# Kernel tuning notes

Measured on AMD Instinct MI355X. Metric: run time of the kernel, lower is better.

## Reference

```python
import jax, jax.numpy as jnp
import numpy as np

N_NODES = 16384   # n_nodes
N_LINKS = 8192    # batch of target links
D_EMB = 128       # embedding dim
EDGE_P = 0.004    # adjacency density -> avg degree ~65


def setup_inputs() -> dict:
    key = jax.random.key(0)
    k1, k2, k3 = jax.random.split(key, 3)
    adj = jax.random.bernoulli(k1, EDGE_P, (N_NODES, N_NODES))
    adj = adj | adj.T                      # symmetric graph
    adj = adj & ~jnp.eye(N_NODES, dtype=bool)  # no self loops
    links = jax.random.randint(k2, (N_LINKS, 2), 0, N_NODES)
    emb = jax.random.normal(k3, (N_NODES, D_EMB), dtype=jnp.float32)
    return {"targetLink": links, "adjacent": adj, "NodeEmbedding": emb}


def reference(targetLink, adjacent, NodeEmbedding):
    # targetLink: [B,2] int, adjacent: [N,N] bool, NodeEmbedding: [N,D] float
    i = targetLink[:, 0]
    j = targetLink[:, 1]
    emb_i = NodeEmbedding[i]               # [B,D] gather
    emb_j = NodeEmbedding[j]               # [B,D] gather
    product = emb_i * emb_j                # [B,D]
    # common-neighbor indicator: u is a CN of (i,j) iff adj[i,u] and adj[j,u]
    cn_mask = (adjacent[i] & adjacent[j]).astype(NodeEmbedding.dtype)  # [B,N]
    # sum of embeddings over common neighbors (fused gather-reduce)
    cn_sum = cn_mask @ NodeEmbedding       # [B,D]
    return jnp.concatenate([product, cn_sum], axis=-1)  # [B,2D]
```

## Files before the change

### kernel.cpp

```cpp
#include <hip/hip_runtime.h>

#define N_NODES 16384
#define D_EMB   128
#define LIST_CAP 1024
#define BM_U64   256
#define FLAG_OFF N_NODES
#define BM_OFF_BYTES (1 << 17)
#define WS_NEEDED (BM_OFF_BYTES + (size_t)N_NODES * (BM_U64 * 8))

__global__ __launch_bounds__(256) void init_kernel(
    const unsigned int* __restrict__ words, int* __restrict__ flags)
{
    if (blockIdx.x < 64) {
        flags[blockIdx.x * 256 + threadIdx.x] = 0;
    } else {
        __shared__ int s_any;
        if (threadIdx.x == 0) s_any = 0;
        __syncthreads();
        int any = 0;
        for (int k = threadIdx.x; k < 16384; k += 256)
            if (words[k] > 1u) any = 1;
        if (any) atomicOr(&s_any, 1);
        __syncthreads();
        if (threadIdx.x == 0) flags[FLAG_OFF] = s_any;
    }
}

__global__ __launch_bounds__(256) void claim_compress_kernel(
    const int* __restrict__ links, const void* __restrict__ adjv,
    int* __restrict__ flags, unsigned long long* __restrict__ bm64,
    int n_endpoints)
{
    const int e = blockIdx.x;
    if (e >= n_endpoints) return;
    const int r = links[e];

    __shared__ int s_claimed;
    if (threadIdx.x == 0)
        s_claimed = (atomicCAS(&flags[r], 0, 1) == 0) ? 1 : 0;
    __syncthreads();
    if (!s_claimed) return;

    const int t = threadIdx.x;
    const int byte_layout = flags[FLAG_OFF];

    if (!byte_layout) {
        const uint4* row = reinterpret_cast<const uint4*>(
            (const int*)adjv + (size_t)r * N_NODES);
        unsigned int lo = 0u, hi = 0u;
#pragma unroll
        for (int k = 0; k < 8; ++k) {
            const uint4 v = row[k * 256 + t];
            const unsigned int nib = min(v.x, 1u) | (min(v.y, 1u) << 1)
                                   | (min(v.z, 1u) << 2) | (min(v.w, 1u) << 3);
            lo |= nib << (4 * k);
        }
#pragma unroll
        for (int k = 8; k < 16; ++k) {
            const uint4 v = row[k * 256 + t];
            const unsigned int nib = min(v.x, 1u) | (min(v.y, 1u) << 1)
                                   | (min(v.z, 1u) << 2) | (min(v.w, 1u) << 3);
            hi |= nib << (4 * (k - 8));
        }
        bm64[(size_t)r * BM_U64 + t] = ((unsigned long long)hi << 32) | lo;
    } else {
        const uint4* row = reinterpret_cast<const uint4*>(
            (const unsigned char*)adjv + (size_t)r * N_NODES);
        unsigned long long bits = 0ull;
#pragma unroll
        for (int q = 0; q < 4; ++q) {
            const uint4 v = row[t * 4 + q];
            const unsigned int arr[4] = {v.x, v.y, v.z, v.w};
#pragma unroll
            for (int a = 0; a < 4; ++a)
#pragma unroll
                for (int bb = 0; bb < 4; ++bb)
                    if ((arr[a] >> (8 * bb)) & 0xFFu)
                        bits |= 1ull << (q * 16 + a * 4 + bb);
        }
        bm64[(size_t)r * BM_U64 + t] = bits;
    }
}

__global__ __launch_bounds__(256) void link_kernel(
    const int* __restrict__ links, const unsigned long long* __restrict__ bm64,
    const float* __restrict__ emb, float* __restrict__ out,
    const int* __restrict__ flags, int n_links)
{
    const int link = blockIdx.x;
    if (link >= n_links) return;
    const int i = links[2 * link];
    const int j = links[2 * link + 1];
    const int byte_layout = flags[FLAG_OFF];

    __shared__ int s_list[LIST_CAP];
    __shared__ int s_count;
    if (threadIdx.x == 0) s_count = 0;
    __syncthreads();

    const int t = threadIdx.x;
    unsigned long long m = bm64[(size_t)i * BM_U64 + t]
                         & bm64[(size_t)j * BM_U64 + t];
    while (m) {
        const int b = __ffsll(m) - 1;
        m &= m - 1;
        const int node = byte_layout
            ? (t * 64 + b)
            : (((b >> 2) << 10) + (t << 2) + (b & 3));
        const int pos = atomicAdd(&s_count, 1);
        if (pos < LIST_CAP) s_list[pos] = node;
    }
    __syncthreads();

    int count = s_count;
    if (count > LIST_CAP) count = LIST_CAP;

    const size_t obase = (size_t)link * (2 * D_EMB);
    if (t < D_EMB) {
        out[obase + t] = emb[(size_t)i * D_EMB + t] * emb[(size_t)j * D_EMB + t];
    } else {
        const int d = t - D_EMB;
        float s = 0.0f;
        for (int c = 0; c < count; ++c)
            s += emb[(size_t)s_list[c] * D_EMB + d];
        out[obase + D_EMB + d] = s;
    }
}

__global__ __launch_bounds__(256) void detect_layout_kernel(
    const unsigned int* __restrict__ words, int* __restrict__ flag)
{
    __shared__ int s_any;
    if (threadIdx.x == 0) s_any = 0;
    __syncthreads();
    int any = 0;
    for (int k = threadIdx.x; k < 16384; k += 256)
        if (words[k] > 1u) any = 1;
    if (any) atomicOr(&s_any, 1);
    __syncthreads();
    if (threadIdx.x == 0) *flag = s_any;
}

__global__ __launch_bounds__(256) void ncn_direct(
    const int* __restrict__ links, const void* __restrict__ adjv,
    const float* __restrict__ emb, float* __restrict__ out,
    const int* __restrict__ flag, int n_links)
{
    const int link = blockIdx.x;
    if (link >= n_links) return;
    const int i = links[2 * link];
    const int j = links[2 * link + 1];

    __shared__ int s_list[LIST_CAP];
    __shared__ int s_count;
    if (threadIdx.x == 0) s_count = 0;
    __syncthreads();

    const int byte_layout = flag ? flag[0] : 0;
    if (byte_layout) {
        const uint4* rowi = reinterpret_cast<const uint4*>(
            (const unsigned char*)adjv + (size_t)i * N_NODES);
        const uint4* rowj = reinterpret_cast<const uint4*>(
            (const unsigned char*)adjv + (size_t)j * N_NODES);
#pragma unroll
        for (int c = 0; c < 4; ++c) {
            const int idx = c * 256 + threadIdx.x;
            const uint4 a = rowi[idx];
            const uint4 bq = rowj[idx];
            unsigned int m[4] = {a.x & bq.x, a.y & bq.y, a.z & bq.z, a.w & bq.w};
            if (m[0] | m[1] | m[2] | m[3]) {
                const int base = idx * 16;
#pragma unroll
                for (int w = 0; w < 4; ++w) {
                    unsigned int v = m[w];
                    if (!v) continue;
#pragma unroll
                    for (int b8 = 0; b8 < 4; ++b8) {
                        if ((v >> (8 * b8)) & 0xFFu) {
                            int pos = atomicAdd(&s_count, 1);
                            if (pos < LIST_CAP) s_list[pos] = base + w * 4 + b8;
                        }
                    }
                }
            }
        }
    } else {
        const uint4* rowi = reinterpret_cast<const uint4*>(
            (const int*)adjv + (size_t)i * N_NODES);
        const uint4* rowj = reinterpret_cast<const uint4*>(
            (const int*)adjv + (size_t)j * N_NODES);
#pragma unroll
        for (int c = 0; c < 16; ++c) {
            const int idx = c * 256 + threadIdx.x;
            const uint4 a = rowi[idx];
            const uint4 bq = rowj[idx];
            const int base = idx * 4;
            if (a.x & bq.x) { int p = atomicAdd(&s_count, 1); if (p < LIST_CAP) s_list[p] = base + 0; }
            if (a.y & bq.y) { int p = atomicAdd(&s_count, 1); if (p < LIST_CAP) s_list[p] = base + 1; }
            if (a.z & bq.z) { int p = atomicAdd(&s_count, 1); if (p < LIST_CAP) s_list[p] = base + 2; }
            if (a.w & bq.w) { int p = atomicAdd(&s_count, 1); if (p < LIST_CAP) s_list[p] = base + 3; }
        }
    }
    __syncthreads();

    int count = s_count;
    if (count > LIST_CAP) count = LIST_CAP;

    const int t = threadIdx.x;
    const size_t obase = (size_t)link * (2 * D_EMB);
    if (t < D_EMB) {
        out[obase + t] = emb[(size_t)i * D_EMB + t] * emb[(size_t)j * D_EMB + t];
    } else {
        const int d = t - D_EMB;
        float s = 0.0f;
        for (int c = 0; c < count; ++c)
            s += emb[(size_t)s_list[c] * D_EMB + d];
        out[obase + D_EMB + d] = s;
    }
}

extern "C" void kernel_launch(void* const* d_in, const int* in_sizes, int n_in,
                              void* d_out, int out_size, void* d_ws, size_t ws_size,
                              hipStream_t stream) {
    const int* links = (const int*)d_in[0];
    const void* adj = d_in[1];
    const float* emb = (const float*)d_in[2];
    float* out = (float*)d_out;

    const int n_links = in_sizes[0] / 2;

    if (ws_size >= WS_NEEDED) {
        int* flags = (int*)d_ws;
        unsigned long long* bm64 =
            (unsigned long long*)((char*)d_ws + BM_OFF_BYTES);

        init_kernel<<<65, 256, 0, stream>>>((const unsigned int*)adj, flags);
        claim_compress_kernel<<<2 * n_links, 256, 0, stream>>>(
            links, adj, flags, bm64, 2 * n_links);
        link_kernel<<<n_links, 256, 0, stream>>>(
            links, bm64, emb, out, flags, n_links);
    } else {
        int* flag = (ws_size >= sizeof(int)) ? (int*)d_ws : nullptr;
        if (flag) detect_layout_kernel<<<1, 256, 0, stream>>>(
            (const unsigned int*)adj, flag);
        ncn_direct<<<n_links, 256, 0, stream>>>(links, adj, emb, out, flag, n_links);
    }
}
```

Before: 178.1 us.

## Compact unique endpoint rows into a list and compress two rows per block

Replaces the per-endpoint claim-and-compress blocks with a thread-level marking kernel that appends unique row IDs to a workspace list. A second kernel then compresses two adjacency rows per block into bitmaps. This removes the many blocks that previously launched only to exit, and doubles the outstanding loads per thread. It adds an extra launch, and blocks beyond the unique count still launch and exit.

```diff
diff --git a/kernel.cpp b/kernel.cpp
--- a/kernel.cpp
+++ b/kernel.cpp
@@ -5,17 +5,19 @@
 #define LIST_CAP 1024
 #define BM_U64   256
 #define FLAG_OFF N_NODES
-#define BM_OFF_BYTES (1 << 17)
+#define CNT_OFF  (N_NODES + 1)
+#define LIST_OFF (N_NODES + 8)
+#define BM_OFF_BYTES (1 << 18)
 #define WS_NEEDED (BM_OFF_BYTES + (size_t)N_NODES * (BM_U64 * 8))
 
-__global__ __launch_bounds__(256) void init_kernel(
+__global__ __launch_bounds__(256) void zero_probe_kernel(
     const unsigned int* __restrict__ words, int* __restrict__ flags)
 {
     if (blockIdx.x < 64) {
         flags[blockIdx.x * 256 + threadIdx.x] = 0;
     } else {
         __shared__ int s_any;
-        if (threadIdx.x == 0) s_any = 0;
+        if (threadIdx.x == 0) { s_any = 0; flags[CNT_OFF] = 0; }
         __syncthreads();
         int any = 0;
         for (int k = threadIdx.x; k < 16384; k += 256)
@@ -26,59 +28,88 @@
     }
 }
 
-__global__ __launch_bounds__(256) void claim_compress_kernel(
-    const int* __restrict__ links, const void* __restrict__ adjv,
-    int* __restrict__ flags, unsigned long long* __restrict__ bm64,
-    int n_endpoints)
-{
-    const int e = blockIdx.x;
+__global__ __launch_bounds__(256) void mark_list_kernel(
+    const int* __restrict__ links, int* __restrict__ flags, int n_endpoints)
+{
+    const int e = blockIdx.x * 256 + threadIdx.x;
     if (e >= n_endpoints) return;
     const int r = links[e];
-
-    __shared__ int s_claimed;
-    if (threadIdx.x == 0)
-        s_claimed = (atomicCAS(&flags[r], 0, 1) == 0) ? 1 : 0;
-    __syncthreads();
-    if (!s_claimed) return;
-
+    if (atomicCAS(&flags[r], 0, 1) == 0) {
+        const int pos = atomicAdd(&flags[CNT_OFF], 1);
+        flags[LIST_OFF + pos] = r;
+    }
+}
+
+__global__ __launch_bounds__(256) void compress_pair_kernel(
+    const void* __restrict__ adjv, const int* __restrict__ flags,
+    unsigned long long* __restrict__ bm64)
+{
+    const int n_used = flags[CNT_OFF];
+    const int i0 = 2 * blockIdx.x;
+    const int i1 = i0 + 1;
+    if (i0 >= n_used) return;
+    const int r0 = flags[LIST_OFF + i0];
+    const int r1 = (i1 < n_used) ? flags[LIST_OFF + i1] : -1;
     const int t = threadIdx.x;
     const int byte_layout = flags[FLAG_OFF];
 
     if (!byte_layout) {
-        const uint4* row = reinterpret_cast<const uint4*>(
-            (const int*)adjv + (size_t)r * N_NODES);
-        unsigned int lo = 0u, hi = 0u;
-#pragma unroll
-        for (int k = 0; k < 8; ++k) {
-            const uint4 v = row[k * 256 + t];
-            const unsigned int nib = min(v.x, 1u) | (min(v.y, 1u) << 1)
-                                   | (min(v.z, 1u) << 2) | (min(v.w, 1u) << 3);
-            lo |= nib << (4 * k);
-        }
-#pragma unroll
-        for (int k = 8; k < 16; ++k) {
-            const uint4 v = row[k * 256 + t];
-            const unsigned int nib = min(v.x, 1u) | (min(v.y, 1u) << 1)
-                                   | (min(v.z, 1u) << 2) | (min(v.w, 1u) << 3);
-            hi |= nib << (4 * (k - 8));
-        }
-        bm64[(size_t)r * BM_U64 + t] = ((unsigned long long)hi << 32) | lo;
-    } else {
-        const uint4* row = reinterpret_cast<const uint4*>(
-            (const unsigned char*)adjv + (size_t)r * N_NODES);
-        unsigned long long bits = 0ull;
-#pragma unroll
-        for (int q = 0; q < 4; ++q) {
-            const uint4 v = row[t * 4 + q];
-            const unsigned int arr[4] = {v.x, v.y, v.z, v.w};
-#pragma unroll
-            for (int a = 0; a < 4; ++a)
-#pragma unroll
-                for (int bb = 0; bb < 4; ++bb)
-                    if ((arr[a] >> (8 * bb)) & 0xFFu)
-                        bits |= 1ull << (q * 16 + a * 4 + bb);
-        }
-        bm64[(size_t)r * BM_U64 + t] = bits;
+        const uint4* rowA = reinterpret_cast<const uint4*>(
+            (const int*)adjv + (size_t)r0 * N_NODES);
+        if (r1 >= 0) {
+            const uint4* rowB = reinterpret_cast<const uint4*>(
+                (const int*)adjv + (size_t)r1 * N_NODES);
+            unsigned int lo0 = 0u, hi0 = 0u, lo1 = 0u, hi1 = 0u;
+#pragma unroll
+            for (int k = 0; k < 8; ++k) {
+                const uint4 a = rowA[k * 256 + t];
+                const uint4 b = rowB[k * 256 + t];
+                lo0 |= (min(a.x,1u) | (min(a.y,1u)<<1) | (min(a.z,1u)<<2) | (min(a.w,1u)<<3)) << (4*k);
+                lo1 |= (min(b.x,1u) | (min(b.y,1u)<<1) | (min(b.z,1u)<<2) | (min(b.w,1u)<<3)) << (4*k);
+            }
+#pragma unroll
+            for (int k = 8; k < 16; ++k) {
+                const uint4 a = rowA[k * 256 + t];
+                const uint4 b = rowB[k * 256 + t];
+                hi0 |= (min(a.x,1u) | (min(a.y,1u)<<1) | (min(a.z,1u)<<2) | (min(a.w,1u)<<3)) << (4*(k-8));
+                hi1 |= (min(b.x,1u) | (min(b.y,1u)<<1) | (min(b.z,1u)<<2) | (min(b.w,1u)<<3)) << (4*(k-8));
+            }
+            bm64[(size_t)r0 * BM_U64 + t] = ((unsigned long long)hi0 << 32) | lo0;
+            bm64[(size_t)r1 * BM_U64 + t] = ((unsigned long long)hi1 << 32) | lo1;
+        } else {
+            unsigned int lo0 = 0u, hi0 = 0u;
+#pragma unroll
+            for (int k = 0; k < 8; ++k) {
+                const uint4 a = rowA[k * 256 + t];
+                lo0 |= (min(a.x,1u) | (min(a.y,1u)<<1) | (min(a.z,1u)<<2) | (min(a.w,1u)<<3)) << (4*k);
+            }
+#pragma unroll
+            for (int k = 8; k < 16; ++k) {
+                const uint4 a = rowA[k * 256 + t];
+                hi0 |= (min(a.x,1u) | (min(a.y,1u)<<1) | (min(a.z,1u)<<2) | (min(a.w,1u)<<3)) << (4*(k-8));
+            }
+            bm64[(size_t)r0 * BM_U64 + t] = ((unsigned long long)hi0 << 32) | lo0;
+        }
+    } else {
+        for (int s = 0; s < 2; ++s) {
+            const int r = (s == 0) ? r0 : r1;
+            if (r < 0) break;
+            const uint4* row = reinterpret_cast<const uint4*>(
+                (const unsigned char*)adjv + (size_t)r * N_NODES);
+            unsigned long long bits = 0ull;
+#pragma unroll
+            for (int q = 0; q < 4; ++q) {
+                const uint4 v = row[t * 4 + q];
+                const unsigned int arr[4] = {v.x, v.y, v.z, v.w};
+#pragma unroll
+                for (int a = 0; a < 4; ++a)
+#pragma unroll
+                    for (int bb = 0; bb < 4; ++bb)
+                        if ((arr[a] >> (8 * bb)) & 0xFFu)
+                            bits |= 1ull << (q * 16 + a * 4 + bb);
+            }
+            bm64[(size_t)r * BM_U64 + t] = bits;
+        }
     }
 }
 
@@ -234,9 +265,12 @@
         unsigned long long* bm64 =
             (unsigned long long*)((char*)d_ws + BM_OFF_BYTES);
 
-        init_kernel<<<65, 256, 0, stream>>>((const unsigned int*)adj, flags);
-        claim_compress_kernel<<<2 * n_links, 256, 0, stream>>>(
-            links, adj, flags, bm64, 2 * n_links);
+        zero_probe_kernel<<<65, 256, 0, stream>>>(
+            (const unsigned int*)adj, flags);
+        mark_list_kernel<<<(2 * n_links + 255) / 256, 256, 0, stream>>>(
+            links, flags, 2 * n_links);
+        compress_pair_kernel<<<N_NODES / 2, 256, 0, stream>>>(
+            adj, flags, bm64);
         link_kernel<<<n_links, 256, 0, stream>>>(
             links, bm64, emb, out, flags, n_links);
     } else {
```

Result: no change. 181.3 us (+1.8%).

## Replace bitmap compression with counting-sort of links by min endpoint for cache reuse

Applied to the files above, without the earlier changes.

Drops the two-pass bitmap path (compress each endpoint's adjacency row to 64-bit words, then intersect). It now counting-sorts links by their smaller endpoint, using a histogram, a scan and a scatter, and intersects the raw adjacency rows directly. Blocks are interleaved across eight chunks of the sorted order so links sharing a row run close together in time and reuse it from L2. This avoids writing and re-reading the bitmap, but each link now reads two full adjacency rows, and only one of the two rows benefits from the sorting.

```diff
diff --git a/kernel.cpp b/kernel.cpp
--- a/kernel.cpp
+++ b/kernel.cpp
@@ -3,16 +3,17 @@
 #define N_NODES 16384
 #define D_EMB   128
 #define LIST_CAP 1024
-#define BM_U64   256
-#define FLAG_OFF N_NODES
-#define BM_OFF_BYTES (1 << 17)
-#define WS_NEEDED (BM_OFF_BYTES + (size_t)N_NODES * (BM_U64 * 8))
-
-__global__ __launch_bounds__(256) void init_kernel(
+#define HIST_OFF 0
+#define FLAG_OFF 16384
+#define CUM_OFF  16448
+#define PERM_OFF 32896
+#define WS_NEEDED ((PERM_OFF + 16384) * sizeof(int))
+
+__global__ __launch_bounds__(256) void zero_probe_kernel(
     const unsigned int* __restrict__ words, int* __restrict__ flags)
 {
     if (blockIdx.x < 64) {
-        flags[blockIdx.x * 256 + threadIdx.x] = 0;
+        flags[HIST_OFF + blockIdx.x * 256 + threadIdx.x] = 0;
     } else {
         __shared__ int s_any;
         if (threadIdx.x == 0) s_any = 0;
@@ -26,137 +27,69 @@
     }
 }
 
-__global__ __launch_bounds__(256) void claim_compress_kernel(
+__global__ __launch_bounds__(256) void count_kernel(
+    const int* __restrict__ links, int* __restrict__ flags, int n_links)
+{
+    const int e = blockIdx.x * 256 + threadIdx.x;
+    if (e >= n_links) return;
+    const int a = min(links[2 * e], links[2 * e + 1]);
+    atomicAdd(&flags[HIST_OFF + a], 1);
+}
+
+__global__ __launch_bounds__(256) void scan_kernel(int* __restrict__ flags)
+{
+    __shared__ int s_part[256];
+    const int t = threadIdx.x;
+    const int base = t * 64;
+    int sum = 0;
+    for (int k = 0; k < 64; ++k) sum += flags[HIST_OFF + base + k];
+    s_part[t] = sum;
+    __syncthreads();
+    if (t == 0) {
+        int acc = 0;
+        for (int k = 0; k < 256; ++k) { int v = s_part[k]; s_part[k] = acc; acc += v; }
+    }
+    __syncthreads();
+    int acc = s_part[t];
+    for (int k = 0; k < 64; ++k) {
+        const int v = flags[HIST_OFF + base + k];
+        flags[CUM_OFF + base + k] = acc;
+        acc += v;
+    }
+}
+
+__global__ __launch_bounds__(256) void scatter_kernel(
+    const int* __restrict__ links, int* __restrict__ flags, int n_links)
+{
+    const int e = blockIdx.x * 256 + threadIdx.x;
+    if (e >= n_links) return;
+    const int a = min(links[2 * e], links[2 * e + 1]);
+    const int pos = atomicAdd(&flags[CUM_OFF + a], 1);
+    flags[PERM_OFF + pos] = e;
+}
+
+__global__ __launch_bounds__(256) void ncn_sorted_kernel(
     const int* __restrict__ links, const void* __restrict__ adjv,
-    int* __restrict__ flags, unsigned long long* __restrict__ bm64,
-    int n_endpoints)
-{
-    const int e = blockIdx.x;
-    if (e >= n_endpoints) return;
-    const int r = links[e];
-
-    __shared__ int s_claimed;
-    if (threadIdx.x == 0)
-        s_claimed = (atomicCAS(&flags[r], 0, 1) == 0) ? 1 : 0;
-    __syncthreads();
-    if (!s_claimed) return;
-
-    const int t = threadIdx.x;
-    const int byte_layout = flags[FLAG_OFF];
-
-    if (!byte_layout) {
-        const uint4* row = reinterpret_cast<const uint4*>(
-            (const int*)adjv + (size_t)r * N_NODES);
-        unsigned int lo = 0u, hi = 0u;
-#pragma unroll
-        for (int k = 0; k < 8; ++k) {
-            const uint4 v = row[k * 256 + t];
-            const unsigned int nib = min(v.x, 1u) | (min(v.y, 1u) << 1)
-                                   | (min(v.z, 1u) << 2) | (min(v.w, 1u) << 3);
-            lo |= nib << (4 * k);
-        }
-#pragma unroll
-        for (int k = 8; k < 16; ++k) {
-            const uint4 v = row[k * 256 + t];
-            const unsigned int nib = min(v.x, 1u) | (min(v.y, 1u) << 1)
-                                   | (min(v.z, 1u) << 2) | (min(v.w, 1u) << 3);
-            hi |= nib << (4 * (k - 8));
-        }
-        bm64[(size_t)r * BM_U64 + t] = ((unsigned long long)hi << 32) | lo;
-    } else {
-        const uint4* row = reinterpret_cast<const uint4*>(
-            (const unsigned char*)adjv + (size_t)r * N_NODES);
-        unsigned long long bits = 0ull;
-#pragma unroll
-        for (int q = 0; q < 4; ++q) {
-            const uint4 v = row[t * 4 + q];
-            const unsigned int arr[4] = {v.x, v.y, v.z, v.w};
-#pragma unroll
-            for (int a = 0; a < 4; ++a)
-#pragma unroll
-                for (int bb = 0; bb < 4; ++bb)
-                    if ((arr[a] >> (8 * bb)) & 0xFFu)
-                        bits |= 1ull << (q * 16 + a * 4 + bb);
-        }
-        bm64[(size_t)r * BM_U64 + t] = bits;
-    }
-}
-
-__global__ __launch_bounds__(256) void link_kernel(
-    const int* __restrict__ links, const unsigned long long* __restrict__ bm64,
     const float* __restrict__ emb, float* __restrict__ out,
     const int* __restrict__ flags, int n_links)
 {
-    const int link = blockIdx.x;
-    if (link >= n_links) return;
-    const int i = links[2 * link];
-    const int j = links[2 * link + 1];
-    const int byte_layout = flags[FLAG_OFF];
+    int b = blockIdx.x;
+    if (b >= n_links) return;
+    int s = b;
+    if ((n_links & 7) == 0) {
+        const int chunk = n_links >> 3;
+        s = (b & 7) * chunk + (b >> 3);
+    }
+    const int lid = flags[PERM_OFF + s];
+    const int i0 = links[2 * lid], j0 = links[2 * lid + 1];
+    const int i = min(i0, j0), j = max(i0, j0);
 
     __shared__ int s_list[LIST_CAP];
     __shared__ int s_count;
     if (threadIdx.x == 0) s_count = 0;
     __syncthreads();
 
-    const int t = threadIdx.x;
-    unsigned long long m = bm64[(size_t)i * BM_U64 + t]
-                         & bm64[(size_t)j * BM_U64 + t];
-    while (m) {
-        const int b = __ffsll(m) - 1;
-        m &= m - 1;
-        const int node = byte_layout
-            ? (t * 64 + b)
-            : (((b >> 2) << 10) + (t << 2) + (b & 3));
-        const int pos = atomicAdd(&s_count, 1);
-        if (pos < LIST_CAP) s_list[pos] = node;
-    }
-    __syncthreads();
-
-    int count = s_count;
-    if (count > LIST_CAP) count = LIST_CAP;
-
-    const size_t obase = (size_t)link * (2 * D_EMB);
-    if (t < D_EMB) {
-        out[obase + t] = emb[(size_t)i * D_EMB + t] * emb[(size_t)j * D_EMB + t];
-    } else {
-        const int d = t - D_EMB;
-        float s = 0.0f;
-        for (int c = 0; c < count; ++c)
-            s += emb[(size_t)s_list[c] * D_EMB + d];
-        out[obase + D_EMB + d] = s;
-    }
-}
-
-__global__ __launch_bounds__(256) void detect_layout_kernel(
-    const unsigned int* __restrict__ words, int* __restrict__ flag)
-{
-    __shared__ int s_any;
-    if (threadIdx.x == 0) s_any = 0;
-    __syncthreads();
-    int any = 0;
-    for (int k = threadIdx.x; k < 16384; k += 256)
-        if (words[k] > 1u) any = 1;
-    if (any) atomicOr(&s_any, 1);
-    __syncthreads();
-    if (threadIdx.x == 0) *flag = s_any;
-}
-
-__global__ __launch_bounds__(256) void ncn_direct(
-    const int* __restrict__ links, const void* __restrict__ adjv,
-    const float* __restrict__ emb, float* __restrict__ out,
-    const int* __restrict__ flag, int n_links)
-{
-    const int link = blockIdx.x;
-    if (link >= n_links) return;
-    const int i = links[2 * link];
-    const int j = links[2 * link + 1];
-
-    __shared__ int s_list[LIST_CAP];
-    __shared__ int s_count;
-    if (threadIdx.x == 0) s_count = 0;
-    __syncthreads();
-
-    const int byte_layout = flag ? flag[0] : 0;
+    const int byte_layout = flags[FLAG_OFF];
     if (byte_layout) {
         const uint4* rowi = reinterpret_cast<const uint4*>(
             (const unsigned char*)adjv + (size_t)i * N_NODES);
@@ -207,6 +140,98 @@
     if (count > LIST_CAP) count = LIST_CAP;
 
     const int t = threadIdx.x;
+    const size_t obase = (size_t)lid * (2 * D_EMB);
+    if (t < D_EMB) {
+        out[obase + t] = emb[(size_t)i * D_EMB + t] * emb[(size_t)j * D_EMB + t];
+    } else {
+        const int d = t - D_EMB;
+        float ssum = 0.0f;
+        for (int c = 0; c < count; ++c)
+            ssum += emb[(size_t)s_list[c] * D_EMB + d];
+        out[obase + D_EMB + d] = ssum;
+    }
+}
+
+__global__ __launch_bounds__(256) void detect_layout_kernel(
+    const unsigned int* __restrict__ words, int* __restrict__ flag)
+{
+    __shared__ int s_any;
+    if (threadIdx.x == 0) s_any = 0;
+    __syncthreads();
+    int any = 0;
+    for (int k = threadIdx.x; k < 16384; k += 256)
+        if (words[k] > 1u) any = 1;
+    if (any) atomicOr(&s_any, 1);
+    __syncthreads();
+    if (threadIdx.x == 0) *flag = s_any;
+}
+
+__global__ __launch_bounds__(256) void ncn_direct(
+    const int* __restrict__ links, const void* __restrict__ adjv,
+    const float* __restrict__ emb, float* __restrict__ out,
+    const int* __restrict__ flag, int n_links)
+{
+    const int link = blockIdx.x;
+    if (link >= n_links) return;
+    const int i = links[2 * link];
+    const int j = links[2 * link + 1];
+
+    __shared__ int s_list[LIST_CAP];
+    __shared__ int s_count;
+    if (threadIdx.x == 0) s_count = 0;
+    __syncthreads();
+
+    const int byte_layout = flag ? flag[0] : 0;
+    if (byte_layout) {
+        const uint4* rowi = reinterpret_cast<const uint4*>(
+            (const unsigned char*)adjv + (size_t)i * N_NODES);
+        const uint4* rowj = reinterpret_cast<const uint4*>(
+            (const unsigned char*)adjv + (size_t)j * N_NODES);
+#pragma unroll
+        for (int c = 0; c < 4; ++c) {
+            const int idx = c * 256 + threadIdx.x;
+            const uint4 a = rowi[idx];
+            const uint4 bq = rowj[idx];
+            unsigned int m[4] = {a.x & bq.x, a.y & bq.y, a.z & bq.z, a.w & bq.w};
+            if (m[0] | m[1] | m[2] | m[3]) {
+                const int base = idx * 16;
+#pragma unroll
+                for (int w = 0; w < 4; ++w) {
+                    unsigned int v = m[w];
+                    if (!v) continue;
+#pragma unroll
+                    for (int b8 = 0; b8 < 4; ++b8) {
+                        if ((v >> (8 * b8)) & 0xFFu) {
+                            int pos = atomicAdd(&s_count, 1);
+                            if (pos < LIST_CAP) s_list[pos] = base + w * 4 + b8;
+                        }
+                    }
+                }
+            }
+        }
+    } else {
+        const uint4* rowi = reinterpret_cast<const uint4*>(
+            (const int*)adjv + (size_t)i * N_NODES);
+        const uint4* rowj = reinterpret_cast<const uint4*>(
+            (const int*)adjv + (size_t)j * N_NODES);
+#pragma unroll
+        for (int c = 0; c < 16; ++c) {
+            const int idx = c * 256 + threadIdx.x;
+            const uint4 a = rowi[idx];
+            const uint4 bq = rowj[idx];
+            const int base = idx * 4;
+            if (a.x & bq.x) { int p = atomicAdd(&s_count, 1); if (p < LIST_CAP) s_list[p] = base + 0; }
+            if (a.y & bq.y) { int p = atomicAdd(&s_count, 1); if (p < LIST_CAP) s_list[p] = base + 1; }
+            if (a.z & bq.z) { int p = atomicAdd(&s_count, 1); if (p < LIST_CAP) s_list[p] = base + 2; }
+            if (a.w & bq.w) { int p = atomicAdd(&s_count, 1); if (p < LIST_CAP) s_list[p] = base + 3; }
+        }
+    }
+    __syncthreads();
+
+    int count = s_count;
+    if (count > LIST_CAP) count = LIST_CAP;
+
+    const int t = threadIdx.x;
     const size_t obase = (size_t)link * (2 * D_EMB);
     if (t < D_EMB) {
         out[obase + t] = emb[(size_t)i * D_EMB + t] * emb[(size_t)j * D_EMB + t];
@@ -229,16 +254,17 @@
 
     const int n_links = in_sizes[0] / 2;
 
-    if (ws_size >= WS_NEEDED) {
+    if (ws_size >= WS_NEEDED && n_links <= 16384) {
         int* flags = (int*)d_ws;
-        unsigned long long* bm64 =
-            (unsigned long long*)((char*)d_ws + BM_OFF_BYTES);
-
-        init_kernel<<<65, 256, 0, stream>>>((const unsigned int*)adj, flags);
-        claim_compress_kernel<<<2 * n_links, 256, 0, stream>>>(
-            links, adj, flags, bm64, 2 * n_links);
-        link_kernel<<<n_links, 256, 0, stream>>>(
-            links, bm64, emb, out, flags, n_links);
+        zero_probe_kernel<<<65, 256, 0, stream>>>(
+            (const unsigned int*)adj, flags);
+        count_kernel<<<(n_links + 255) / 256, 256, 0, stream>>>(
+            links, flags, n_links);
+        scan_kernel<<<1, 256, 0, stream>>>(flags);
+        scatter_kernel<<<(n_links + 255) / 256, 256, 0, stream>>>(
+            links, flags, n_links);
+        ncn_sorted_kernel<<<n_links, 256, 0, stream>>>(
+            links, adj, emb, out, flags, n_links);
     } else {
         int* flag = (ws_size >= sizeof(int)) ? (int*)d_ws : nullptr;
         if (flag) detect_layout_kernel<<<1, 256, 0, stream>>>(
```

After: 180.8 us. No clear change (+1.6%).
